# Kernel optimization log

Measured on AMD Instinct MI355X. Metric: run time of the kernel, lower is better.

The kernel has to match this reference:

```python
import jax, jax.numpy as jnp
import numpy as np

TAU = 0.95

def _f1_per_position(labels):
    # labels: [B, L] binary relevance. r[b, j] = F1 if the list is truncated at position j+1.
    B, L = labels.shape
    csum = jnp.cumsum(labels, axis=1)                       # [B, L] relevant docs kept at cutoff k=j+1
    k = jnp.arange(1, L + 1, dtype=labels.dtype)            # [L]
    total = jnp.sum(labels, axis=1, keepdims=True)          # [B, 1] total relevant per list
    prec = csum / k
    rec = jnp.where(total > 0, csum / jnp.maximum(total, 1.0), 0.0)
    denom = prec + rec
    return jnp.where(denom > 0, 2.0 * prec * rec / jnp.maximum(denom, 1e-20), 0.0)


def setup_inputs() -> dict:
    key = jax.random.key(0)
    k1, k2 = jax.random.split(key)
    B, L = 8192, 2048
    # output: per-position truncation probabilities in (0, 1); log() is applied in the loss.
    output = jax.random.uniform(k1, (B, L, 1), dtype=jnp.float32, minval=1e-4, maxval=1.0)
    labels = jax.random.randint(k2, (B, L), 0, 2).astype(jnp.float32)
    return {"output": output, "labels": labels}


def reference(output, labels):
    # output: [B, L, 1], labels: [B, L]
    B = output.shape[0]
    r = _f1_per_position(labels)                             # [B, L]
    # q = exp(r/tau) / sum_j exp(r/tau)  ==  softmax(r/tau) along positions
    q = jax.nn.softmax(r / TAU, axis=1)
    log_out = jnp.log(output[..., 0])                        # [B, L]
    return -jnp.sum(log_out * q) / B
```

## Files before the change

kernel.cpp:

```cpp
#include <hip/hip_runtime.h>


constexpr int L   = 2048;
constexpr int TPB = 256;
constexpr float TAU   = 0.95f;
constexpr float LOG2E = 1.4426950408889634f;
constexpr float LN2   = 0.6931471805599453f;

__global__ __launch_bounds__(TPB) void attncut_row_kernel(
    const float* __restrict__ output,
    const float* __restrict__ labels,
    float* __restrict__ rowloss,
    int B)
{
    const int wave = threadIdx.x >> 6;
    const int lane = threadIdx.x & 63;
    const int row  = blockIdx.x * 4 + wave;

    const float4* lab4 = reinterpret_cast<const float4*>(labels + (size_t)row * L) + lane;
    const float4* out4 = reinterpret_cast<const float4*>(output + (size_t)row * L) + lane;

    unsigned nibs = 0u;
#pragma unroll
    for (int c = 0; c < 8; ++c) {
        float4 a = lab4[c * 64];
        unsigned b = (unsigned)a.x | ((unsigned)a.y << 1)
                   | ((unsigned)a.z << 2) | ((unsigned)a.w << 3);
        nibs |= b << (4 * c);
    }

    unsigned w[4];
#pragma unroll
    for (int q = 0; q < 4; ++q) {
        unsigned c0 = __popc((nibs >> (8 * q)) & 0xFu);
        unsigned c1 = __popc((nibs >> (8 * q + 4)) & 0xFu);
        w[q] = c0 | (c1 << 16);
    }

#pragma unroll
    for (int d = 1; d < 64; d <<= 1) {
#pragma unroll
        for (int q = 0; q < 4; ++q) {
            unsigned n = __shfl_up(w[q], d, 64);
            if (lane >= d) w[q] += n;
        }
    }

    float T[8], E[8];
#pragma unroll
    for (int q = 0; q < 4; ++q) {
        unsigned tw = __shfl(w[q], 63, 64);
        unsigned own0 = __popc((nibs >> (8 * q)) & 0xFu);
        unsigned own1 = __popc((nibs >> (8 * q + 4)) & 0xFu);
        T[2 * q]     = (float)(tw & 0xFFFFu);
        T[2 * q + 1] = (float)(tw >> 16);
        E[2 * q]     = (float)((w[q] & 0xFFFFu) - own0);
        E[2 * q + 1] = (float)((w[q] >> 16) - own1);
    }
    const float total = ((T[0] + T[1]) + (T[2] + T[3])) + ((T[4] + T[5]) + (T[6] + T[7]));

    const float K2 = (total > 0.f) ? (2.f * LOG2E / TAU) : 0.f;

    float Z = 0.f, Wd = 0.f;
    float off = 0.f;
#pragma unroll
    for (int c = 0; c < 8; ++c) {
        float4 ov = out4[c * 64];
        float cf = off + E[c];
        const unsigned nib = (nibs >> (4 * c)) & 0xFu;
        const float kb = total + (float)(c * 256 + 4 * lane);

        cf += (float)(nib & 1u);
        float e0 = __builtin_amdgcn_exp2f((K2 * cf) * __builtin_amdgcn_rcpf(kb + 1.f));
        Z += e0;  Wd = fmaf(__builtin_amdgcn_logf(ov.x), e0, Wd);

        cf += (float)((nib >> 1) & 1u);
        float e1 = __builtin_amdgcn_exp2f((K2 * cf) * __builtin_amdgcn_rcpf(kb + 2.f));
        Z += e1;  Wd = fmaf(__builtin_amdgcn_logf(ov.y), e1, Wd);

        cf += (float)((nib >> 2) & 1u);
        float e2 = __builtin_amdgcn_exp2f((K2 * cf) * __builtin_amdgcn_rcpf(kb + 3.f));
        Z += e2;  Wd = fmaf(__builtin_amdgcn_logf(ov.z), e2, Wd);

        cf += (float)((nib >> 3) & 1u);
        float e3 = __builtin_amdgcn_exp2f((K2 * cf) * __builtin_amdgcn_rcpf(kb + 4.f));
        Z += e3;  Wd = fmaf(__builtin_amdgcn_logf(ov.w), e3, Wd);

        off += T[c];
    }

#pragma unroll
    for (int d = 32; d; d >>= 1) {
        Z  += __shfl_xor(Z, d, 64);
        Wd += __shfl_xor(Wd, d, 64);
    }
    if (lane == 0) rowloss[row] = -LN2 * Wd / Z;
}

__global__ __launch_bounds__(TPB) void attncut_reduce_kernel(
    const float* __restrict__ rowloss, float* __restrict__ out, int B)
{
    const int t = threadIdx.x;
    const float4* r4 = reinterpret_cast<const float4*>(rowloss);
    float s = 0.f;
    for (int i = t; i < B / 4; i += TPB) {
        float4 v = r4[i];
        s += (v.x + v.y) + (v.z + v.w);
    }
#pragma unroll
    for (int d = 32; d; d >>= 1) s += __shfl_xor(s, d, 64);
    __shared__ float ws[4];
    if ((t & 63) == 0) ws[t >> 6] = s;
    __syncthreads();
    if (t == 0) out[0] = (ws[0] + ws[1] + ws[2] + ws[3]) / (float)B;
}

extern "C" void kernel_launch(void* const* d_in, const int* in_sizes, int n_in,
                              void* d_out, int out_size, void* d_ws, size_t ws_size,
                              hipStream_t stream) {
    const float* output = (const float*)d_in[0];
    const float* labels = (const float*)d_in[1];
    const int B = in_sizes[1] / L;

    float* rowloss = (float*)d_ws;

    attncut_row_kernel<<<B / 4, TPB, 0, stream>>>(output, labels, rowloss, B);
    attncut_reduce_kernel<<<1, TPB, 0, stream>>>(rowloss, (float*)d_out, B);
}
```

Measured before the change: 28.69 us.

## Fuse row loss and final reduction with atomics and hoist all row loads

Removes the second reduction kernel by having each block sum its four row losses in shared memory and atomically add the scaled partial to the output, which is zeroed with a memset beforehand. All label and output vectors for a row are now loaded up front, labels with nontemporal hints, so more memory requests are in flight before compute begins. A launch-bounds occupancy hint is added as well. The cost is higher register pressure, many atomics on a single address, and a float sum whose order is no longer deterministic.

Result: slower. 43.83 us (+52.8%).

```diff
diff --git a/kernel.cpp b/kernel.cpp
--- a/kernel.cpp
+++ b/kernel.cpp
@@ -7,25 +7,32 @@
 constexpr float LOG2E = 1.4426950408889634f;
 constexpr float LN2   = 0.6931471805599453f;
 
-__global__ __launch_bounds__(TPB) void attncut_row_kernel(
+typedef float f32x4 __attribute__((ext_vector_type(4)));
+
+__global__ __launch_bounds__(TPB, 4) void attncut_fused_kernel(
     const float* __restrict__ output,
     const float* __restrict__ labels,
-    float* __restrict__ rowloss,
-    int B)
+    float* __restrict__ loss,
+    float invB)
 {
     const int wave = threadIdx.x >> 6;
     const int lane = threadIdx.x & 63;
     const int row  = blockIdx.x * 4 + wave;
 
-    const float4* lab4 = reinterpret_cast<const float4*>(labels + (size_t)row * L) + lane;
-    const float4* out4 = reinterpret_cast<const float4*>(output + (size_t)row * L) + lane;
+    const f32x4* lab4 = reinterpret_cast<const f32x4*>(labels + (size_t)row * L) + lane;
+    const f32x4* out4 = reinterpret_cast<const f32x4*>(output + (size_t)row * L) + lane;
+
+    f32x4 lb[8], ov[8];
+#pragma unroll
+    for (int c = 0; c < 8; ++c) lb[c] = __builtin_nontemporal_load(lab4 + c * 64);
+#pragma unroll
+    for (int c = 0; c < 8; ++c) ov[c] = out4[c * 64];
 
     unsigned nibs = 0u;
 #pragma unroll
     for (int c = 0; c < 8; ++c) {
-        float4 a = lab4[c * 64];
-        unsigned b = (unsigned)a.x | ((unsigned)a.y << 1)
-                   | ((unsigned)a.z << 2) | ((unsigned)a.w << 3);
+        unsigned b = (unsigned)lb[c][0] | ((unsigned)lb[c][1] << 1)
+                   | ((unsigned)lb[c][2] << 2) | ((unsigned)lb[c][3] << 3);
         nibs |= b << (4 * c);
     }
 
@@ -65,26 +72,25 @@
     float off = 0.f;
 #pragma unroll
     for (int c = 0; c < 8; ++c) {
-        float4 ov = out4[c * 64];
         float cf = off + E[c];
         const unsigned nib = (nibs >> (4 * c)) & 0xFu;
         const float kb = total + (float)(c * 256 + 4 * lane);
 
         cf += (float)(nib & 1u);
         float e0 = __builtin_amdgcn_exp2f((K2 * cf) * __builtin_amdgcn_rcpf(kb + 1.f));
-        Z += e0;  Wd = fmaf(__builtin_amdgcn_logf(ov.x), e0, Wd);
+        Z += e0;  Wd = fmaf(__builtin_amdgcn_logf(ov[c][0]), e0, Wd);
 
         cf += (float)((nib >> 1) & 1u);
         float e1 = __builtin_amdgcn_exp2f((K2 * cf) * __builtin_amdgcn_rcpf(kb + 2.f));
-        Z += e1;  Wd = fmaf(__builtin_amdgcn_logf(ov.y), e1, Wd);
+        Z += e1;  Wd = fmaf(__builtin_amdgcn_logf(ov[c][1]), e1, Wd);
 
         cf += (float)((nib >> 2) & 1u);
         float e2 = __builtin_amdgcn_exp2f((K2 * cf) * __builtin_amdgcn_rcpf(kb + 3.f));
-        Z += e2;  Wd = fmaf(__builtin_amdgcn_logf(ov.z), e2, Wd);
+        Z += e2;  Wd = fmaf(__builtin_amdgcn_logf(ov[c][2]), e2, Wd);
 
         cf += (float)((nib >> 3) & 1u);
         float e3 = __builtin_amdgcn_exp2f((K2 * cf) * __builtin_amdgcn_rcpf(kb + 4.f));
-        Z += e3;  Wd = fmaf(__builtin_amdgcn_logf(ov.w), e3, Wd);
+        Z += e3;  Wd = fmaf(__builtin_amdgcn_logf(ov[c][3]), e3, Wd);
 
         off += T[c];
     }
@@ -94,25 +100,14 @@
         Z  += __shfl_xor(Z, d, 64);
         Wd += __shfl_xor(Wd, d, 64);
     }
-    if (lane == 0) rowloss[row] = -LN2 * Wd / Z;
-}
 
-__global__ __launch_bounds__(TPB) void attncut_reduce_kernel(
-    const float* __restrict__ rowloss, float* __restrict__ out, int B)
-{
-    const int t = threadIdx.x;
-    const float4* r4 = reinterpret_cast<const float4*>(rowloss);
-    float s = 0.f;
-    for (int i = t; i < B / 4; i += TPB) {
-        float4 v = r4[i];
-        s += (v.x + v.y) + (v.z + v.w);
+    __shared__ float part[4];
+    if (lane == 0) part[wave] = -LN2 * Wd / Z;
+    __syncthreads();
+    if (threadIdx.x == 0) {
+        float p = (part[0] + part[1]) + (part[2] + part[3]);
+        atomicAdd(loss, p * invB);
     }
-#pragma unroll
-    for (int d = 32; d; d >>= 1) s += __shfl_xor(s, d, 64);
-    __shared__ float ws[4];
-    if ((t & 63) == 0) ws[t >> 6] = s;
-    __syncthreads();
-    if (t == 0) out[0] = (ws[0] + ws[1] + ws[2] + ws[3]) / (float)B;
 }
 
 extern "C" void kernel_launch(void* const* d_in, const int* in_sizes, int n_in,
@@ -122,8 +117,7 @@
     const float* labels = (const float*)d_in[1];
     const int B = in_sizes[1] / L;
 
-    float* rowloss = (float*)d_ws;
-
-    attncut_row_kernel<<<B / 4, TPB, 0, stream>>>(output, labels, rowloss, B);
-    attncut_reduce_kernel<<<1, TPB, 0, stream>>>(rowloss, (float*)d_out, B);
+    hipMemsetAsync(d_out, 0, sizeof(float), stream);
+    attncut_fused_kernel<<<B / 4, TPB, 0, stream>>>(output, labels,
+                                                    (float*)d_out, 1.0f / (float)B);
 }
```
